# Kernel tuning notes

Measured on AMD Instinct MI355X. Metric: run time of the kernel, lower is better.

## Reference

```python
import jax, jax.numpy as jnp
import numpy as np

E = 256   # embed_dim
H = 8     # num_heads
D = E // H  # head_dim = 32
L = 1024  # seq len (Q_len == K_len == V_len)


def setup_inputs() -> dict:
    key = jax.random.key(0)
    ks = jax.random.split(key, 10)
    f = lambda k, s: jax.random.normal(k, s, dtype=jnp.float32)
    return {
        "V": f(ks[0], (L, E)),
        "K": f(ks[1], (L, E)),
        "Q": f(ks[2], (L, E)),
        # genomic-style coordinates, strictly positive
        "position": jax.random.uniform(ks[3], (L,), dtype=jnp.float32) * 1e5,
        "Wq": f(ks[4], (E, E)) * 0.02,
        "Wk": f(ks[5], (E, E)) * 0.02,
        "Wv": f(ks[6], (E, E)) * 0.02,
        "Wr": f(ks[7], (E, 1)) * 0.02,   # K_relative_linear weight [out=E, in=1]
        "Wo": f(ks[8], (E, E)) * 0.02,
        "bo": jnp.zeros((E,), jnp.float32),
    }


def reference(V, K, Q, position, Wq, Wk, Wv, Wr, Wo, bo):
    Lq = Q.shape[0]
    # projections (nn.Linear: x @ W.T), split into heads -> (L, H, D)
    q = (Q @ Wq.T).reshape(Lq, H, D)
    k = (K @ Wk.T).reshape(Lq, H, D)
    v = (V @ Wv.T).reshape(Lq, H, D)

    # relative position scalar per (q, k) pair: log(|p_q - p_k| + 1)
    rel = jnp.log(jnp.abs(position[:, None] - position[None, :]) + 1.0)  # (L, L)

    # K_relative_linear maps scalar rel -> (H, D); the einsum
    # 'nqhd,nhqjd->nhqj' then factorizes exactly as:
    #   sum_d Q[q,h,d] * rel[q,j] * Wr[h,d] = (Q . Wr)[h,q] * rel[q,j]
    # so we avoid materializing the (H, L, L, D) tensor while computing
    # mathematically identical results.
    Wr_h = Wr[:, 0].reshape(H, D)                    # (H, D)
    coeff = jnp.einsum('qhd,hd->hq', q, Wr_h)        # (H, L)

    energy = jnp.einsum('qhd,khd->hqk', q, k)        # (H, L, L)
    energy = energy + coeff[:, :, None] * rel[None, :, :]

    attn = jax.nn.softmax(energy / np.float32(E) ** 0.5, axis=2)
    out = jnp.einsum('hqk,khd->qhd', attn, v).reshape(Lq, E)
    out = out @ Wo.T + bo
    return out
```

## Files before the change

### kernel.cpp

```cpp
#include <hip/hip_runtime.h>
#include <math.h>

#define EDIM 256
#define LDIM 1024
#define HDIM 8
#define DDIM 32

typedef __attribute__((ext_vector_type(8))) short short8;
typedef __attribute__((ext_vector_type(4))) float f32x4;

__device__ inline unsigned short bf16h(float x) {
    unsigned u = __float_as_uint(x);
    return (unsigned short)((u + 0x7fff + ((u >> 16) & 1)) >> 16);
}
__device__ inline float bf16tof(unsigned short h) {
    return __uint_as_float(((unsigned)h) << 16);
}

__global__ __launch_bounds__(256) void proj_kernel(
    const float* __restrict__ Q, const float* __restrict__ Km, const float* __restrict__ V,
    const float* __restrict__ Wq, const float* __restrict__ Wk, const float* __restrict__ Wv,
    const float* __restrict__ Wr,
    float* __restrict__ qT, float* __restrict__ kT, float* __restrict__ vT,
    float* __restrict__ coeff)
{
    const int z = blockIdx.z;
    const float* __restrict__ X = (z == 0) ? Q : (z == 1) ? Km : V;
    const float* __restrict__ W = (z == 0) ? Wq : (z == 1) ? Wk : Wv;
    float* __restrict__ dst     = (z == 0) ? qT : (z == 1) ? kT : vT;

    const int n0 = blockIdx.x * 32;
    const int o0 = blockIdx.y * 32;
    const int tid = threadIdx.x;
    const int tx = tid & 15, ty = tid >> 4;

    __shared__ float Xs[32][34];
    __shared__ float Ws[32][34];

    float acc[2][2] = {{0.f,0.f},{0.f,0.f}};

    const int sn  = tid >> 3;
    const int sc4 = (tid & 7) * 4;

    float4 xa = *(const float4*)(X + (n0 + sn) * EDIM + sc4);
    float4 wa = *(const float4*)(W + (o0 + sn) * EDIM + sc4);

    for (int kb = 0; kb < EDIM; kb += 32) {
        __syncthreads();
        Xs[sc4+0][sn]=xa.x; Xs[sc4+1][sn]=xa.y; Xs[sc4+2][sn]=xa.z; Xs[sc4+3][sn]=xa.w;
        Ws[sc4+0][sn]=wa.x; Ws[sc4+1][sn]=wa.y; Ws[sc4+2][sn]=wa.z; Ws[sc4+3][sn]=wa.w;
        float4 xn, wn;
        if (kb + 32 < EDIM) {
            xn = *(const float4*)(X + (n0 + sn) * EDIM + kb + 32 + sc4);
            wn = *(const float4*)(W + (o0 + sn) * EDIM + kb + 32 + sc4);
        }
        __syncthreads();
        #pragma unroll
        for (int e = 0; e < 32; ++e) {
            float2 x2 = *(const float2*)&Xs[e][ty*2];
            float2 w2 = *(const float2*)&Ws[e][tx*2];
            acc[0][0] += x2.x*w2.x; acc[0][1] += x2.x*w2.y;
            acc[1][0] += x2.y*w2.x; acc[1][1] += x2.y*w2.y;
        }
        xa = xn; wa = wn;
    }

    const int h = o0 >> 5;
    #pragma unroll
    for (int i = 0; i < 2; ++i) {
        const int n = n0 + ty*2 + i;
        float2 r; r.x = acc[i][0]; r.y = acc[i][1];
        *(float2*)(dst + h*(LDIM*DDIM) + n*DDIM + tx*2) = r;
    }

    if (z == 0) {
        const float wr0 = Wr[o0 + tx*2], wr1 = Wr[o0 + tx*2 + 1];
        #pragma unroll
        for (int i = 0; i < 2; ++i) {
            float c = acc[i][0]*wr0 + acc[i][1]*wr1;
            c += __shfl_xor(c, 1, 64);
            c += __shfl_xor(c, 2, 64);
            c += __shfl_xor(c, 4, 64);
            c += __shfl_xor(c, 8, 64);
            if (tx == 0) coeff[h*LDIM + n0 + ty*2 + i] = c;
        }
    }
}

__global__ __launch_bounds__(256, 4) void attn_kernel(
    const float* __restrict__ qT, const float* __restrict__ kT, const float* __restrict__ vT,
    const float* __restrict__ coeff, const float* __restrict__ pos,
    float* __restrict__ Op, float* __restrict__ Mp, float* __restrict__ Lp, int nkt)
{
    const int h   = blockIdx.y;
    const int q0  = blockIdx.x * 64;
    const int p   = blockIdx.z;
    const int kt0 = p * nkt * 64;
    const int tid  = threadIdx.x;
    const int wave = tid >> 6;
    const int lane = tid & 63;
    const int n    = lane & 15;
    const int quad = lane >> 4;
    const int qs0  = wave * 16;

    __shared__ __align__(16) short khi[4*64*8];
    __shared__ __align__(16) short klo[4*64*8];
    __shared__ float vs[64][36];
    __shared__ float ps_t[64][68];
    __shared__ float alph[64];
    __shared__ float pk[64];

    short8 qhi, qlo;
    {
        const float* qp = qT + (h*LDIM + q0 + qs0 + n) * DDIM + quad*8;
        float4 qa = *(const float4*)qp;
        float4 qb = *(const float4*)(qp + 4);
        float v[8] = {qa.x,qa.y,qa.z,qa.w, qb.x,qb.y,qb.z,qb.w};
        #pragma unroll
        for (int j = 0; j < 8; ++j) {
            unsigned short hh = bf16h(v[j]);
            qhi[j] = (short)hh;
            qlo[j] = (short)bf16h(v[j] - bf16tof(hh));
        }
    }

    float pq[4], cq[4];
    #pragma unroll
    for (int i = 0; i < 4; ++i) {
        const int r = q0 + qs0 + 4*quad + i;
        pq[i] = pos[r];
        cq[i] = coeff[h*LDIM + r] * 0.0625f;
    }

    float m[4], l[4];
    #pragma unroll
    for (int i = 0; i < 4; ++i) { m[i] = -INFINITY; l[i] = 0.f; }

    const int pr0 = (tid >> 4) * 4;
    const int dg2 = (tid & 15) * 2;
    float o[4][2];
    #pragma unroll
    for (int i = 0; i < 4; ++i) { o[i][0] = 0.f; o[i][1] = 0.f; }

    const int cS = tid >> 2;
    const int dq = tid & 3;
    const int lane2 = (cS & 15) | (dq << 4);
    const int gS = cS >> 4;

    float4 k0c, k1c, v0c, v1c; float pkc = 0.f;
    {
        const float* kp = kT + (h*LDIM + kt0 + cS) * DDIM + dq*8;
        k0c = *(const float4*)kp; k1c = *(const float4*)(kp + 4);
        const float* vp = vT + (h*LDIM + kt0 + cS) * DDIM + dq*8;
        v0c = *(const float4*)vp; v1c = *(const float4*)(vp + 4);
        if (tid < 64) pkc = pos[kt0 + tid];
    }

    for (int t = 0; t < nkt; ++t) {
        __syncthreads();

        {
            float kv[8] = {k0c.x,k0c.y,k0c.z,k0c.w, k1c.x,k1c.y,k1c.z,k1c.w};
            short8 hi8, lo8;
            #pragma unroll
            for (int j = 0; j < 8; ++j) {
                unsigned short hh = bf16h(kv[j]);
                hi8[j] = (short)hh;
                lo8[j] = (short)bf16h(kv[j] - bf16tof(hh));
            }
            *((short8*)&khi[(gS*64 + lane2)*8]) = hi8;
            *((short8*)&klo[(gS*64 + lane2)*8]) = lo8;
            *(float4*)&vs[cS][dq*8]     = v0c;
            *(float4*)&vs[cS][dq*8 + 4] = v1c;
            if (tid < 64) pk[tid] = pkc;
        }

        float4 k0n, k1n, v0n, v1n; float pkn = 0.f;
        if (t + 1 < nkt) {
            const int kt = kt0 + (t+1) * 64;
            const float* kp = kT + (h*LDIM + kt + cS) * DDIM + dq*8;
            k0n = *(const float4*)kp; k1n = *(const float4*)(kp + 4);
            const float* vp = vT + (h*LDIM + kt + cS) * DDIM + dq*8;
            v0n = *(const float4*)vp; v1n = *(const float4*)(vp + 4);
            if (tid < 64) pkn = pos[kt + tid];
        }
        __syncthreads();

        f32x4 Sf[4];
        #pragma unroll
        for (int t4 = 0; t4 < 4; ++t4) {
            short8 bhi = *((const short8*)&khi[(t4*64 + lane)*8]);
            short8 blo = *((const short8*)&klo[(t4*64 + lane)*8]);
            f32x4 acc = {0.f, 0.f, 0.f, 0.f};
            acc = __builtin_amdgcn_mfma_f32_16x16x32_bf16(qlo, bhi, acc, 0, 0, 0);
            acc = __builtin_amdgcn_mfma_f32_16x16x32_bf16(qhi, blo, acc, 0, 0, 0);
            acc = __builtin_amdgcn_mfma_f32_16x16x32_bf16(qhi, bhi, acc, 0, 0, 0);
            Sf[t4] = acc;
        }

        float ev[4][4];
        float rmax[4] = {-INFINITY, -INFINITY, -INFINITY, -INFINITY};
        #pragma unroll
        for (int t4 = 0; t4 < 4; ++t4) {
            const float pkt = pk[16*t4 + n];
            #pragma unroll
            for (int i = 0; i < 4; ++i) {
                float s = fmaf(Sf[t4][i], 0.0625f, cq[i] * __logf(fabsf(pq[i] - pkt) + 1.f));
                ev[t4][i] = s;
                rmax[i] = fmaxf(rmax[i], s);
            }
        }
        #pragma unroll
        for (int off = 1; off < 16; off <<= 1)
            #pragma unroll
            for (int i = 0; i < 4; ++i)
                rmax[i] = fmaxf(rmax[i], __shfl_xor(rmax[i], off, 64));

        float al[4], rsum[4];
        #pragma unroll
        for (int i = 0; i < 4; ++i) {
            const float mn = fmaxf(m[i], rmax[i]);
            al[i] = __expf(m[i] - mn);
            m[i] = mn;
            rsum[i] = 0.f;
        }
        #pragma unroll
        for (int t4 = 0; t4 < 4; ++t4)
            #pragma unroll
            for (int i = 0; i < 4; ++i) {
                float e = __expf(ev[t4][i] - m[i]);
                ev[t4][i] = e;
                rsum[i] += e;
            }
        #pragma unroll
        for (int off = 1; off < 16; off <<= 1)
            #pragma unroll
            for (int i = 0; i < 4; ++i)
                rsum[i] += __shfl_xor(rsum[i], off, 64);
        #pragma unroll
        for (int i = 0; i < 4; ++i) l[i] = l[i]*al[i] + rsum[i];

        if (n == 0) {
            #pragma unroll
            for (int i = 0; i < 4; ++i) alph[qs0 + 4*quad + i] = al[i];
        }
        #pragma unroll
        for (int t4 = 0; t4 < 4; ++t4) {
            float4 w; w.x = ev[t4][0]; w.y = ev[t4][1]; w.z = ev[t4][2]; w.w = ev[t4][3];
            *(float4*)&ps_t[16*t4 + n][qs0 + 4*quad] = w;
        }
        __syncthreads();

        {
            float4 a4 = *(const float4*)&alph[pr0];
            o[0][0]*=a4.x; o[0][1]*=a4.x; o[1][0]*=a4.y; o[1][1]*=a4.y;
            o[2][0]*=a4.z; o[2][1]*=a4.z; o[3][0]*=a4.w; o[3][1]*=a4.w;
        }
        #pragma unroll 4
        for (int c = 0; c < 64; ++c) {
            float4 p4 = *(const float4*)&ps_t[c][pr0];
            float2 v2 = *(const float2*)&vs[c][dg2];
            o[0][0] += p4.x*v2.x; o[0][1] += p4.x*v2.y;
            o[1][0] += p4.y*v2.x; o[1][1] += p4.y*v2.y;
            o[2][0] += p4.z*v2.x; o[2][1] += p4.z*v2.y;
            o[3][0] += p4.w*v2.x; o[3][1] += p4.w*v2.y;
        }

        k0c = k0n; k1c = k1n; v0c = v0n; v1c = v1n; pkc = pkn;
    }

    const int ph = p * HDIM + h;
    #pragma unroll
    for (int i = 0; i < 4; ++i) {
        float2 w; w.x = o[i][0]; w.y = o[i][1];
        *(float2*)(Op + ((size_t)ph*LDIM + q0 + pr0 + i)*DDIM + dg2) = w;
    }
    if (n == 0) {
        #pragma unroll
        for (int i = 0; i < 4; ++i) {
            const int r = q0 + qs0 + 4*quad + i;
            Mp[ph*LDIM + r] = m[i];
            Lp[ph*LDIM + r] = l[i];
        }
    }
}

__global__ __launch_bounds__(256) void combine_kernel(
    const float* __restrict__ Op, const float* __restrict__ Mp, const float* __restrict__ Lp,
    int P, float* __restrict__ A)
{
    const int idx = blockIdx.x * 256 + threadIdx.x;
    const int n  = idx >> 6;
    const int e4 = (idx & 63) * 4;
    const int h  = e4 >> 5;
    const int d  = e4 & 31;

    float mv[8], lv[8];
    float mx = -INFINITY;
    #pragma unroll
    for (int p = 0; p < 8; ++p) if (p < P) {
        mv[p] = Mp[(p*HDIM + h)*LDIM + n];
        lv[p] = Lp[(p*HDIM + h)*LDIM + n];
        mx = fmaxf(mx, mv[p]);
    }
    float s = 0.f;
    #pragma unroll
    for (int p = 0; p < 8; ++p) if (p < P) {
        float a = __expf(mv[p] - mx);
        mv[p] = a;
        s += a * lv[p];
    }
    const float inv = 1.f / s;

    float4 x; x.x = x.y = x.z = x.w = 0.f;
    #pragma unroll
    for (int p = 0; p < 8; ++p) if (p < P) {
        const float sp = mv[p] * inv;
        float4 xp = *(const float4*)(Op + ((size_t)(p*HDIM + h)*LDIM + n)*DDIM + d);
        x.x += sp*xp.x; x.y += sp*xp.y; x.z += sp*xp.z; x.w += sp*xp.w;
    }
    *(float4*)(A + n*EDIM + e4) = x;
}

__global__ __launch_bounds__(256) void outproj_kernel(
    const float* __restrict__ A, const float* __restrict__ Wo,
    const float* __restrict__ bo, float* __restrict__ out)
{
    const int n0 = blockIdx.x * 32;
    const int o0 = blockIdx.y * 32;
    const int tid = threadIdx.x;
    const int tx = tid & 15, ty = tid >> 4;

    __shared__ float Xs[32][34];
    __shared__ float Ws[32][34];

    float acc[2][2] = {{0.f,0.f},{0.f,0.f}};

    const int sn  = tid >> 3;
    const int sc4 = (tid & 7) * 4;

    float4 xa = *(const float4*)(A  + (n0 + sn) * EDIM + sc4);
    float4 wa = *(const float4*)(Wo + (o0 + sn) * EDIM + sc4);

    for (int kb = 0; kb < EDIM; kb += 32) {
        __syncthreads();
        Xs[sc4+0][sn]=xa.x; Xs[sc4+1][sn]=xa.y; Xs[sc4+2][sn]=xa.z; Xs[sc4+3][sn]=xa.w;
        Ws[sc4+0][sn]=wa.x; Ws[sc4+1][sn]=wa.y; Ws[sc4+2][sn]=wa.z; Ws[sc4+3][sn]=wa.w;
        float4 xn, wn;
        if (kb + 32 < EDIM) {
            xn = *(const float4*)(A  + (n0 + sn) * EDIM + kb + 32 + sc4);
            wn = *(const float4*)(Wo + (o0 + sn) * EDIM + kb + 32 + sc4);
        }
        __syncthreads();
        #pragma unroll
        for (int e = 0; e < 32; ++e) {
            float2 x2 = *(const float2*)&Xs[e][ty*2];
            float2 w2 = *(const float2*)&Ws[e][tx*2];
            acc[0][0] += x2.x*w2.x; acc[0][1] += x2.x*w2.y;
            acc[1][0] += x2.y*w2.x; acc[1][1] += x2.y*w2.y;
        }
        xa = xn; wa = wn;
    }

    const int oo = o0 + tx*2;
    float2 bias = *(const float2*)(bo + oo);
    #pragma unroll
    for (int i = 0; i < 2; ++i) {
        const int nn = n0 + ty*2 + i;
        float2 r; r.x = acc[i][0] + bias.x; r.y = acc[i][1] + bias.y;
        *(float2*)(out + nn*EDIM + oo) = r;
    }
}

extern "C" void kernel_launch(void* const* d_in, const int* in_sizes, int n_in,
                              void* d_out, int out_size, void* d_ws, size_t ws_size,
                              hipStream_t stream) {
    const float* V   = (const float*)d_in[0];
    const float* K   = (const float*)d_in[1];
    const float* Q   = (const float*)d_in[2];
    const float* pos = (const float*)d_in[3];
    const float* Wq  = (const float*)d_in[4];
    const float* Wk  = (const float*)d_in[5];
    const float* Wv  = (const float*)d_in[6];
    const float* Wr  = (const float*)d_in[7];
    const float* Wo  = (const float*)d_in[8];
    const float* bo  = (const float*)d_in[9];
    float* out = (float*)d_out;
    float* ws  = (float*)d_ws;

    auto need = [](int P) -> size_t {
        return (size_t)(794624 + P*278528) * 4;
    };
    int P = 2;
    if (ws_size >= need(8)) P = 8;
    else if (ws_size >= need(4)) P = 4;

    float* qT    = ws;
    float* kT    = ws + 262144;
    float* vT    = ws + 524288;
    float* coeff = ws + 786432;
    float* Op    = ws + 794624;
    float* Mp    = Op + (size_t)P * 262144;
    float* Lp    = Mp + (size_t)P * 8192;
    float* A     = qT;

    proj_kernel   <<<dim3(32, 8, 3), 256, 0, stream>>>(Q, K, V, Wq, Wk, Wv, Wr, qT, kT, vT, coeff);
    attn_kernel   <<<dim3(16, 8, P), 256, 0, stream>>>(qT, kT, vT, coeff, pos, Op, Mp, Lp, 16 / P);
    combine_kernel<<<dim3(256),      256, 0, stream>>>(Op, Mp, Lp, P, A);
    outproj_kernel<<<dim3(32, 8),    256, 0, stream>>>(A, Wo, bo, out);
}
```

Before: 122.0 us.

## Compute P·V with split-bf16 MFMA instead of scalar FMA loop

Replaces the scalar FP32 P·V accumulation with bf16 MFMA 16x16x32 instructions using a hi/lo split (three MFMAs per tile) to keep near-FP32 accuracy. P and V are stored in shared memory as packed hi|lo words in a transposed layout. Each wave now handles its own rows, which removes the alpha shared array and one __syncthreads per tile. The hi part of the split now uses truncation instead of rounding. This trades scalar FMA work and a barrier for extra packing and unpacking work plus different LDS layouts, which may cause bank conflicts.

```diff
diff --git a/kernel.cpp b/kernel.cpp
--- a/kernel.cpp
+++ b/kernel.cpp
@@ -8,6 +8,7 @@
 
 typedef __attribute__((ext_vector_type(8))) short short8;
 typedef __attribute__((ext_vector_type(4))) float f32x4;
+typedef __attribute__((ext_vector_type(4))) unsigned u32x4;
 
 __device__ inline unsigned short bf16h(float x) {
     unsigned u = __float_as_uint(x);
@@ -15,6 +16,11 @@
 }
 __device__ inline float bf16tof(unsigned short h) {
     return __uint_as_float(((unsigned)h) << 16);
+}
+__device__ inline unsigned packsplit(float x) {
+    unsigned u = __float_as_uint(x);
+    float r = x - __uint_as_float(u & 0xffff0000u);
+    return (u & 0xffff0000u) | (unsigned)bf16h(r);
 }
 
 __global__ __launch_bounds__(256) void proj_kernel(
@@ -105,9 +111,8 @@
 
     __shared__ __align__(16) short khi[4*64*8];
     __shared__ __align__(16) short klo[4*64*8];
-    __shared__ float vs[64][36];
-    __shared__ float ps_t[64][68];
-    __shared__ float alph[64];
+    __shared__ __align__(16) unsigned vs2[32][68];
+    __shared__ __align__(16) unsigned pA[64][68];
     __shared__ float pk[64];
 
     short8 qhi, qlo;
@@ -118,9 +123,9 @@
         float v[8] = {qa.x,qa.y,qa.z,qa.w, qb.x,qb.y,qb.z,qb.w};
         #pragma unroll
         for (int j = 0; j < 8; ++j) {
-            unsigned short hh = bf16h(v[j]);
-            qhi[j] = (short)hh;
-            qlo[j] = (short)bf16h(v[j] - bf16tof(hh));
+            unsigned u = __float_as_uint(v[j]);
+            qhi[j] = (short)(u >> 16);
+            qlo[j] = (short)bf16h(v[j] - __uint_as_float(u & 0xffff0000u));
         }
     }
 
@@ -136,11 +141,7 @@
     #pragma unroll
     for (int i = 0; i < 4; ++i) { m[i] = -INFINITY; l[i] = 0.f; }
 
-    const int pr0 = (tid >> 4) * 4;
-    const int dg2 = (tid & 15) * 2;
-    float o[4][2];
-    #pragma unroll
-    for (int i = 0; i < 4; ++i) { o[i][0] = 0.f; o[i][1] = 0.f; }
+    f32x4 of0 = {0.f,0.f,0.f,0.f}, of1 = {0.f,0.f,0.f,0.f};
 
     const int cS = tid >> 2;
     const int dq = tid & 3;
@@ -164,14 +165,16 @@
             short8 hi8, lo8;
             #pragma unroll
             for (int j = 0; j < 8; ++j) {
-                unsigned short hh = bf16h(kv[j]);
-                hi8[j] = (short)hh;
-                lo8[j] = (short)bf16h(kv[j] - bf16tof(hh));
+                unsigned u = __float_as_uint(kv[j]);
+                hi8[j] = (short)(u >> 16);
+                lo8[j] = (short)bf16h(kv[j] - __uint_as_float(u & 0xffff0000u));
             }
             *((short8*)&khi[(gS*64 + lane2)*8]) = hi8;
             *((short8*)&klo[(gS*64 + lane2)*8]) = lo8;
-            *(float4*)&vs[cS][dq*8]     = v0c;
-            *(float4*)&vs[cS][dq*8 + 4] = v1c;
+            float vv[8] = {v0c.x,v0c.y,v0c.z,v0c.w, v1c.x,v1c.y,v1c.z,v1c.w};
+            #pragma unroll
+            for (int j = 0; j < 8; ++j)
+                vs2[dq*8 + j][cS] = packsplit(vv[j]);
             if (tid < 64) pk[tid] = pkc;
         }
 
@@ -229,8 +232,8 @@
             #pragma unroll
             for (int i = 0; i < 4; ++i) {
                 float e = __expf(ev[t4][i] - m[i]);
-                ev[t4][i] = e;
                 rsum[i] += e;
+                pA[qs0 + 4*quad + i][16*t4 + n] = packsplit(e);
             }
         #pragma unroll
         for (int off = 1; off < 16; off <<= 1)
@@ -240,40 +243,53 @@
         #pragma unroll
         for (int i = 0; i < 4; ++i) l[i] = l[i]*al[i] + rsum[i];
 
-        if (n == 0) {
-            #pragma unroll
-            for (int i = 0; i < 4; ++i) alph[qs0 + 4*quad + i] = al[i];
-        }
-        #pragma unroll
-        for (int t4 = 0; t4 < 4; ++t4) {
-            float4 w; w.x = ev[t4][0]; w.y = ev[t4][1]; w.z = ev[t4][2]; w.w = ev[t4][3];
-            *(float4*)&ps_t[16*t4 + n][qs0 + 4*quad] = w;
-        }
-        __syncthreads();
-
-        {
-            float4 a4 = *(const float4*)&alph[pr0];
-            o[0][0]*=a4.x; o[0][1]*=a4.x; o[1][0]*=a4.y; o[1][1]*=a4.y;
-            o[2][0]*=a4.z; o[2][1]*=a4.z; o[3][0]*=a4.w; o[3][1]*=a4.w;
-        }
-        #pragma unroll 4
-        for (int c = 0; c < 64; ++c) {
-            float4 p4 = *(const float4*)&ps_t[c][pr0];
-            float2 v2 = *(const float2*)&vs[c][dg2];
-            o[0][0] += p4.x*v2.x; o[0][1] += p4.x*v2.y;
-            o[1][0] += p4.y*v2.x; o[1][1] += p4.y*v2.y;
-            o[2][0] += p4.z*v2.x; o[2][1] += p4.z*v2.y;
-            o[3][0] += p4.w*v2.x; o[3][1] += p4.w*v2.y;
+        #pragma unroll
+        for (int i = 0; i < 4; ++i) { of0[i] *= al[i]; of1[i] *= al[i]; }
+
+        #pragma unroll
+        for (int ch = 0; ch < 2; ++ch) {
+            const unsigned* ap = &pA[qs0 + n][ch*32 + quad*8];
+            u32x4 a0 = *(const u32x4*)ap;
+            u32x4 a1 = *(const u32x4*)(ap + 4);
+            short8 phi, plo;
+            #pragma unroll
+            for (int j = 0; j < 4; ++j) {
+                phi[j]   = (short)(a0[j] >> 16);
+                plo[j]   = (short)(a0[j] & 0xffffu);
+                phi[j+4] = (short)(a1[j] >> 16);
+                plo[j+4] = (short)(a1[j] & 0xffffu);
+            }
+            #pragma unroll
+            for (int dt = 0; dt < 2; ++dt) {
+                const unsigned* vp = &vs2[dt*16 + n][ch*32 + quad*8];
+                u32x4 b0 = *(const u32x4*)vp;
+                u32x4 b1 = *(const u32x4*)(vp + 4);
+                short8 vhi, vlo;
+                #pragma unroll
+                for (int j = 0; j < 4; ++j) {
+                    vhi[j]   = (short)(b0[j] >> 16);
+                    vlo[j]   = (short)(b0[j] & 0xffffu);
+                    vhi[j+4] = (short)(b1[j] >> 16);
+                    vlo[j+4] = (short)(b1[j] & 0xffffu);
+                }
+                f32x4& of = dt ? of1 : of0;
+                of = __builtin_amdgcn_mfma_f32_16x16x32_bf16(plo, vhi, of, 0, 0, 0);
+                of = __builtin_amdgcn_mfma_f32_16x16x32_bf16(phi, vlo, of, 0, 0, 0);
+                of = __builtin_amdgcn_mfma_f32_16x16x32_bf16(phi, vhi, of, 0, 0, 0);
+            }
         }
 
         k0c = k0n; k1c = k1n; v0c = v0n; v1c = v1n; pkc = pkn;
     }
 
     const int ph = p * HDIM + h;
-    #pragma unroll
-    for (int i = 0; i < 4; ++i) {
-        float2 w; w.x = o[i][0]; w.y = o[i][1];
-        *(float2*)(Op + ((size_t)ph*LDIM + q0 + pr0 + i)*DDIM + dg2) = w;
+    {
+        const size_t base = ((size_t)ph * LDIM + q0 + qs0) * DDIM;
+        #pragma unroll
+        for (int i = 0; i < 4; ++i) {
+            Op[base + (size_t)(4*quad + i)*DDIM + n]      = of0[i];
+            Op[base + (size_t)(4*quad + i)*DDIM + 16 + n] = of1[i];
+        }
     }
     if (n == 0) {
         #pragma unroll
```

Result: faster. 117.7 us (-3.6%).
